# Performance work log

Hardware: AMD Instinct MI355X
Metric: run time of the kernel (lower is better)

Reference implementation:

```python
import jax, jax.numpy as jnp
import numpy as np

NEG_INF = -1e30


def setup_inputs() -> dict:
    key = jax.random.key(0)
    ks = jax.random.split(key, 8)
    B, N, I, O, H = 8, 1024, 64, 32, 4
    return {
        "x": jax.random.normal(ks[0], (B, N, I), dtype=jnp.float32),
        "adj": jax.random.randint(ks[1], (N, N), 0, 2, dtype=jnp.int32),
        "source_prior": jax.random.normal(ks[2], (B, N), dtype=jnp.float32),
        "beta": jax.random.normal(ks[3], (H,), dtype=jnp.float32),
        "weight": jax.random.normal(ks[4], (H, I, O), dtype=jnp.float32) * (1.0 / np.sqrt(I)),
        "attn_src": jax.random.normal(ks[5], (H, O), dtype=jnp.float32) * (1.0 / np.sqrt(O)),
        "attn_dst": jax.random.normal(ks[6], (H, O), dtype=jnp.float32) * (1.0 / np.sqrt(O)),
        "bias": jnp.zeros((H, O), dtype=jnp.float32),
    }


def reference(x, adj, source_prior, beta, weight, attn_src, attn_dst, bias):
    B, N, _ = x.shape
    H, _, O = weight.shape
    # Per-head projection + bias: [B,H,N,O]
    projected = jnp.einsum('bni,hio->bhno', x, weight) + bias[None, :, None, :]
    src_scores = jnp.einsum('bhnd,hd->bhn', projected, attn_src)  # [B,H,N]
    dst_scores = jnp.einsum('bhnd,hd->bhn', projected, attn_dst)  # [B,H,N]
    # Additive attention logits: [B,H,dst,src]
    logits = jax.nn.leaky_relu(dst_scores[..., :, None] + src_scores[..., None, :],
                               negative_slope=0.2)
    # Source-prior correction
    gain = jax.nn.softplus(beta).reshape(1, H, 1, 1)
    logits = logits + gain * source_prior[:, None, None, :]
    # Masked softmax over sources; fully-masked rows stay zero
    mask = (adj != 0)[None, None, :, :]  # [1,1,N,N]
    masked = jnp.where(mask, logits, NEG_INF)
    row_max = jnp.max(masked, axis=-1, keepdims=True)
    row_max = jnp.where(jnp.isfinite(row_max) & (row_max > NEG_INF / 2),
                        row_max, jnp.zeros_like(row_max))
    exp_logits = jnp.where(mask, jnp.exp(logits - row_max), 0.0)
    eps = jnp.finfo(logits.dtype).eps
    denom = jnp.maximum(jnp.sum(exp_logits, axis=-1, keepdims=True), eps)
    attention = exp_logits / denom  # [B,H,N,N]
    # Weighted aggregation: [B,H,N,O]
    output = jnp.einsum('bhij,bhjd->bhid', attention, projected)
    # concat=True: [B,N,H*O]
    encoded = jnp.transpose(output, (0, 2, 1, 3)).reshape(B, N, H * O)
    return encoded
```

## Files before the change

### kernel.cpp

```cpp
#include <hip/hip_runtime.h>
#include <math.h>

#define NB 8
#define NN 1024
#define NI 64
#define NO 32
#define NH 4
#define NEGINF (-1e30f)

typedef _Float16 half8 __attribute__((ext_vector_type(8)));
typedef _Float16 half4v __attribute__((ext_vector_type(4)));
typedef float floatx4 __attribute__((ext_vector_type(4)));

__global__ __launch_bounds__(256) void k_pack(const int* __restrict__ adj,
                                              unsigned char* __restrict__ adjb) {
    const int i = blockIdx.x * 256 + threadIdx.x;
    const int4 v = ((const int4*)adj)[i];
    unsigned int p = (v.x ? 1u : 0u) | ((v.y ? 1u : 0u) << 8) |
                     ((v.z ? 1u : 0u) << 16) | ((v.w ? 1u : 0u) << 24);
    ((unsigned int*)adjb)[i] = p;
}

__global__ __launch_bounds__(256) void k_proj(
    const float* __restrict__ x, const float* __restrict__ beta,
    const float* __restrict__ weight, const float* __restrict__ attn_src,
    const float* __restrict__ attn_dst, const float* __restrict__ bias,
    const float* __restrict__ prior,
    _Float16* __restrict__ projT,
    float* __restrict__ src_s, float* __restrict__ dst_s, float* __restrict__ gp)
{
    __shared__ __align__(16) float xs[32 * 64];
    __shared__ __align__(16) float ws[4 * 64 * 36];
    const int t = threadIdx.x;
    const int ntile = blockIdx.x, b = blockIdx.y;
    const int n0b = ntile * 32;
    {
        const float4* xsrc = (const float4*)(x + ((size_t)b * NN + n0b) * NI);
        float4* xd = (float4*)xs;
        xd[t] = xsrc[t];
        xd[t + 256] = xsrc[t + 256];
    }
    #pragma unroll
    for (int k = 0; k < 8; ++k) {
        int e = t + k * 256;
        int h = e >> 9, rem = e & 511, i = rem >> 3, o4 = rem & 7;
        float4 wv = *(const float4*)(weight + (h * NI + i) * NO + o4 * 4);
        *(float4*)&ws[h * 2304 + i * 36 + o4 * 4] = wv;
    }
    __syncthreads();

    const int o4 = t & 7, h = (t >> 3) & 3, ng = t >> 5;
    const int o0 = o4 * 4, nl0 = ng * 4;
    float acc[4][4];
    #pragma unroll
    for (int kn = 0; kn < 4; ++kn)
        #pragma unroll
        for (int oo = 0; oo < 4; ++oo) acc[kn][oo] = 0.f;

    #pragma unroll 4
    for (int i = 0; i < NI; ++i) {
        const float4 wv = *(const float4*)&ws[h * 2304 + i * 36 + o0];
        #pragma unroll
        for (int kn = 0; kn < 4; ++kn) {
            const float xv = xs[(nl0 + kn) * 64 + i];
            acc[kn][0] = fmaf(xv, wv.x, acc[kn][0]);
            acc[kn][1] = fmaf(xv, wv.y, acc[kn][1]);
            acc[kn][2] = fmaf(xv, wv.z, acc[kn][2]);
            acc[kn][3] = fmaf(xv, wv.w, acc[kn][3]);
        }
    }
    const float4 bv  = *(const float4*)(bias + h * NO + o0);
    const float4 asv = *(const float4*)(attn_src + h * NO + o0);
    const float4 adv = *(const float4*)(attn_dst + h * NO + o0);
    const int bh = b * NH + h;
    float ssum[4], dsum[4];
    #pragma unroll
    for (int kn = 0; kn < 4; ++kn) {
        acc[kn][0] += bv.x; acc[kn][1] += bv.y;
        acc[kn][2] += bv.z; acc[kn][3] += bv.w;
        ssum[kn] = acc[kn][0]*asv.x + acc[kn][1]*asv.y + acc[kn][2]*asv.z + acc[kn][3]*asv.w;
        dsum[kn] = acc[kn][0]*adv.x + acc[kn][1]*adv.y + acc[kn][2]*adv.z + acc[kn][3]*adv.w;
    }
    #pragma unroll
    for (int oo = 0; oo < 4; ++oo) {
        half4v hv;
        hv[0] = (_Float16)acc[0][oo]; hv[1] = (_Float16)acc[1][oo];
        hv[2] = (_Float16)acc[2][oo]; hv[3] = (_Float16)acc[3][oo];
        *(half4v*)(projT + ((size_t)(bh * NO + o0 + oo)) * NN + n0b + nl0) = hv;
    }
    #pragma unroll
    for (int msk = 1; msk <= 4; msk <<= 1) {
        #pragma unroll
        for (int kn = 0; kn < 4; ++kn) {
            ssum[kn] += __shfl_xor(ssum[kn], msk, 64);
            dsum[kn] += __shfl_xor(dsum[kn], msk, 64);
        }
    }
    if (o4 == 0) {
        const float bx = beta[h];
        const float sp = fmaxf(bx, 0.f) + log1pf(__expf(-fabsf(bx)));
        #pragma unroll
        for (int kn = 0; kn < 4; ++kn) {
            const int n = n0b + nl0 + kn;
            src_s[bh * NN + n] = ssum[kn];
            dst_s[bh * NN + n] = dsum[kn];
            gp[bh * NN + n] = sp * prior[b * NN + n];
        }
    }
}

#define VTP 1032

__global__ __launch_bounds__(256) void k_attn(
    const unsigned char* __restrict__ adjb,
    const _Float16* __restrict__ projT,
    const float* __restrict__ src_s, const float* __restrict__ dst_s,
    const float* __restrict__ gp,
    float* __restrict__ out)
{
    __shared__ __align__(16) _Float16 vt[NO * VTP];
    __shared__ __align__(16) float srcs[NN];
    __shared__ __align__(16) float gps[NN];
    __shared__ float pmax[64 * 4];
    const int t = threadIdx.x;
    const int lane = t & 63, wave = t >> 6;
    const int dtile = blockIdx.x, h = blockIdx.y, b = blockIdx.z;
    const int bh = b * NH + h;

    ((float4*)srcs)[t] = ((const float4*)(src_s + bh * NN))[t];
    ((float4*)gps)[t]  = ((const float4*)(gp + bh * NN))[t];
    const _Float16* ptrow = projT + (size_t)bh * NO * NN;
    #pragma unroll
    for (int k = 0; k < 16; ++k) {
        const int e = t + k * 256;
        const int o = e >> 7, sc8 = e & 127;
        *(half8*)&vt[o * VTP + sc8 * 8] =
            *(const half8*)(ptrow + (size_t)o * NN + sc8 * 8);
    }
    __syncthreads();

    {
        const int dl = lane, qt = wave;
        const int drow = dtile * 64 + dl;
        const float dv = dst_s[bh * NN + drow];
        const unsigned char* ar = adjb + (size_t)drow * NN + qt * 256;
        float mx = NEGINF;
        #pragma unroll 4
        for (int k = 0; k < 16; ++k) {
            const uint4 a4 = *(const uint4*)(ar + k * 16);
            const unsigned int wv[4] = {a4.x, a4.y, a4.z, a4.w};
            const int sb = qt * 256 + k * 16;
            #pragma unroll
            for (int w = 0; w < 4; ++w) {
                #pragma unroll
                for (int byi = 0; byi < 4; ++byi) {
                    const int s = sb + w * 4 + byi;
                    const float ts = dv + srcs[s];
                    const float sc = fmaxf(ts, 0.f) + 0.2f * fminf(ts, 0.f) + gps[s];
                    const bool on = (wv[w] >> (8 * byi)) & 1;
                    mx = fmaxf(mx, on ? sc : NEGINF);
                }
            }
        }
        pmax[dl * 4 + qt] = mx;
    }
    __syncthreads();

    const int m = lane & 15, quad = lane >> 4;
    const int d = dtile * 64 + wave * 16 + m;
    const float dreg = dst_s[bh * NN + d];
    const int pmb = (wave * 16 + m) * 4;
    const float rmx = fmaxf(fmaxf(pmax[pmb], pmax[pmb + 1]),
                            fmaxf(pmax[pmb + 2], pmax[pmb + 3]));
    const float rmc = (rmx > -1e29f) ? rmx : 0.f;
    const unsigned char* adjr = adjb + (size_t)d * NN;

    floatx4 acc0 = {0.f, 0.f, 0.f, 0.f}, acc1 = {0.f, 0.f, 0.f, 0.f};
    float psum = 0.f;
    uint2 apre = *(const uint2*)(adjr + quad * 8);

    for (int st = 0; st < 32; ++st) {
        const uint2 acur = apre;
        if (st < 31) apre = *(const uint2*)(adjr + (st + 1) * 32 + quad * 8);
        const int sg = st * 32 + quad * 8;
        float sv[8], gv[8];
        *(float4*)&sv[0] = *(const float4*)&srcs[sg];
        *(float4*)&sv[4] = *(const float4*)&srcs[sg + 4];
        *(float4*)&gv[0] = *(const float4*)&gps[sg];
        *(float4*)&gv[4] = *(const float4*)&gps[sg + 4];
        half8 af;
        #pragma unroll
        for (int j = 0; j < 8; ++j) {
            const unsigned int bit =
                ((j < 4 ? (acur.x >> (8 * j)) : (acur.y >> (8 * (j - 4)))) & 1u);
            const float ts = dreg + sv[j];
            const float lk = fmaxf(ts, 0.f) + 0.2f * fminf(ts, 0.f);
            const float sce = bit ? (lk + gv[j]) : NEGINF;
            const float p = __expf(sce - rmc);
            psum += p;
            af[j] = (_Float16)p;
        }
        const half8 b0 = *(const half8*)&vt[m * VTP + sg];
        const half8 b1 = *(const half8*)&vt[(16 + m) * VTP + sg];
        acc0 = __builtin_amdgcn_mfma_f32_16x16x32_f16(af, b0, acc0, 0, 0, 0);
        acc1 = __builtin_amdgcn_mfma_f32_16x16x32_f16(af, b1, acc1, 0, 0, 0);
    }
    psum += __shfl_xor(psum, 16, 64);
    psum += __shfl_xor(psum, 32, 64);

    #pragma unroll
    for (int r = 0; r < 4; ++r) {
        const int row = quad * 4 + r;
        const float lr = __shfl(psum, row, 64);
        const float inv = 1.f / fmaxf(lr, 1.1920929e-07f);
        float* go = out + ((size_t)(b * NN + dtile * 64 + wave * 16 + row)) * (NH * NO) + h * NO;
        go[m] = acc0[r] * inv;
        go[16 + m] = acc1[r] * inv;
    }
}

extern "C" void kernel_launch(void* const* d_in, const int* in_sizes, int n_in,
                              void* d_out, int out_size, void* d_ws, size_t ws_size,
                              hipStream_t stream) {
    (void)in_sizes; (void)n_in; (void)out_size; (void)ws_size;
    const float* x        = (const float*)d_in[0];
    const int*   adj      = (const int*)d_in[1];
    const float* prior    = (const float*)d_in[2];
    const float* beta     = (const float*)d_in[3];
    const float* weight   = (const float*)d_in[4];
    const float* attn_src = (const float*)d_in[5];
    const float* attn_dst = (const float*)d_in[6];
    const float* bias     = (const float*)d_in[7];
    float* out = (float*)d_out;

    _Float16* projT = (_Float16*)d_ws;
    float* src_s = (float*)((char*)d_ws + (1 << 21));
    float* dst_s = src_s + NB * NH * NN;
    float* gpb   = dst_s + NB * NH * NN;
    unsigned char* adjb = (unsigned char*)(gpb + NB * NH * NN);

    hipLaunchKernelGGL(k_pack, dim3(1024), dim3(256), 0, stream, adj, adjb);
    hipLaunchKernelGGL(k_proj, dim3(32, 8), dim3(256), 0, stream,
                       x, beta, weight, attn_src, attn_dst, bias, prior,
                       projT, src_s, dst_s, gpb);
    hipLaunchKernelGGL(k_attn, dim3(16, 4, 8), dim3(256), 0, stream,
                       adjb, projT, src_s, dst_s, gpb, out);
}
```

Before: 110.0 us.

## Fuse pack, projection and attention into one cooperative kernel with analytic row max

Merges the three kernels into a single cooperative launch of 512 blocks that packs adj, computes the projection, does a grid-wide sync, then runs the attention aggregation with a shared-memory union. The per-row masked max pass is replaced by an upper bound leaky(dst+max src)+max gp, which removes a full adjacency scan. Scores are pre-scaled by log2e so exp2f can be used. This cuts launch overhead and the extra max pass, at the cost of a grid sync and possible underflow if the bound is far above the true row max.

```diff
diff --git a/kernel.cpp b/kernel.cpp
--- a/kernel.cpp
+++ b/kernel.cpp
@@ -1,221 +1,198 @@
 #include <hip/hip_runtime.h>
+#include <hip/hip_cooperative_groups.h>
 #include <math.h>
+
+namespace cg = cooperative_groups;
 
 #define NB 8
 #define NN 1024
 #define NI 64
 #define NO 32
 #define NH 4
-#define NEGINF (-1e30f)
+#define LOG2E 1.4426950408889634f
 
 typedef _Float16 half8 __attribute__((ext_vector_type(8)));
-typedef _Float16 half4v __attribute__((ext_vector_type(4)));
+typedef _Float16 half2v __attribute__((ext_vector_type(2)));
 typedef float floatx4 __attribute__((ext_vector_type(4)));
 
-__global__ __launch_bounds__(256) void k_pack(const int* __restrict__ adj,
-                                              unsigned char* __restrict__ adjb) {
-    const int i = blockIdx.x * 256 + threadIdx.x;
-    const int4 v = ((const int4*)adj)[i];
-    unsigned int p = (v.x ? 1u : 0u) | ((v.y ? 1u : 0u) << 8) |
-                     ((v.z ? 1u : 0u) << 16) | ((v.w ? 1u : 0u) << 24);
-    ((unsigned int*)adjb)[i] = p;
-}
-
-__global__ __launch_bounds__(256) void k_proj(
-    const float* __restrict__ x, const float* __restrict__ beta,
+#define VTP 1032
+
+union SMem {
+    struct { float xs[16 * 64]; float ws[4 * 64 * 36]; } a;
+    struct { _Float16 vt[NO * VTP]; float srcs[NN]; float gps[NN]; float red[16]; } b;
+};
+
+__global__ __launch_bounds__(256, 2) void k_fused(
+    const float* __restrict__ x, const int* __restrict__ adj,
+    const float* __restrict__ prior, const float* __restrict__ beta,
     const float* __restrict__ weight, const float* __restrict__ attn_src,
     const float* __restrict__ attn_dst, const float* __restrict__ bias,
-    const float* __restrict__ prior,
     _Float16* __restrict__ projT,
-    float* __restrict__ src_s, float* __restrict__ dst_s, float* __restrict__ gp)
-{
-    __shared__ __align__(16) float xs[32 * 64];
-    __shared__ __align__(16) float ws[4 * 64 * 36];
-    const int t = threadIdx.x;
-    const int ntile = blockIdx.x, b = blockIdx.y;
-    const int n0b = ntile * 32;
-    {
-        const float4* xsrc = (const float4*)(x + ((size_t)b * NN + n0b) * NI);
-        float4* xd = (float4*)xs;
-        xd[t] = xsrc[t];
-        xd[t + 256] = xsrc[t + 256];
-    }
-    #pragma unroll
-    for (int k = 0; k < 8; ++k) {
-        int e = t + k * 256;
-        int h = e >> 9, rem = e & 511, i = rem >> 3, o4 = rem & 7;
-        float4 wv = *(const float4*)(weight + (h * NI + i) * NO + o4 * 4);
-        *(float4*)&ws[h * 2304 + i * 36 + o4 * 4] = wv;
-    }
-    __syncthreads();
-
-    const int o4 = t & 7, h = (t >> 3) & 3, ng = t >> 5;
-    const int o0 = o4 * 4, nl0 = ng * 4;
-    float acc[4][4];
-    #pragma unroll
-    for (int kn = 0; kn < 4; ++kn)
-        #pragma unroll
-        for (int oo = 0; oo < 4; ++oo) acc[kn][oo] = 0.f;
-
-    #pragma unroll 4
-    for (int i = 0; i < NI; ++i) {
-        const float4 wv = *(const float4*)&ws[h * 2304 + i * 36 + o0];
-        #pragma unroll
-        for (int kn = 0; kn < 4; ++kn) {
-            const float xv = xs[(nl0 + kn) * 64 + i];
-            acc[kn][0] = fmaf(xv, wv.x, acc[kn][0]);
-            acc[kn][1] = fmaf(xv, wv.y, acc[kn][1]);
-            acc[kn][2] = fmaf(xv, wv.z, acc[kn][2]);
-            acc[kn][3] = fmaf(xv, wv.w, acc[kn][3]);
-        }
-    }
-    const float4 bv  = *(const float4*)(bias + h * NO + o0);
-    const float4 asv = *(const float4*)(attn_src + h * NO + o0);
-    const float4 adv = *(const float4*)(attn_dst + h * NO + o0);
-    const int bh = b * NH + h;
-    float ssum[4], dsum[4];
-    #pragma unroll
-    for (int kn = 0; kn < 4; ++kn) {
-        acc[kn][0] += bv.x; acc[kn][1] += bv.y;
-        acc[kn][2] += bv.z; acc[kn][3] += bv.w;
-        ssum[kn] = acc[kn][0]*asv.x + acc[kn][1]*asv.y + acc[kn][2]*asv.z + acc[kn][3]*asv.w;
-        dsum[kn] = acc[kn][0]*adv.x + acc[kn][1]*adv.y + acc[kn][2]*adv.z + acc[kn][3]*adv.w;
-    }
-    #pragma unroll
-    for (int oo = 0; oo < 4; ++oo) {
-        half4v hv;
-        hv[0] = (_Float16)acc[0][oo]; hv[1] = (_Float16)acc[1][oo];
-        hv[2] = (_Float16)acc[2][oo]; hv[3] = (_Float16)acc[3][oo];
-        *(half4v*)(projT + ((size_t)(bh * NO + o0 + oo)) * NN + n0b + nl0) = hv;
-    }
-    #pragma unroll
-    for (int msk = 1; msk <= 4; msk <<= 1) {
-        #pragma unroll
-        for (int kn = 0; kn < 4; ++kn) {
-            ssum[kn] += __shfl_xor(ssum[kn], msk, 64);
-            dsum[kn] += __shfl_xor(dsum[kn], msk, 64);
-        }
-    }
-    if (o4 == 0) {
-        const float bx = beta[h];
-        const float sp = fmaxf(bx, 0.f) + log1pf(__expf(-fabsf(bx)));
-        #pragma unroll
-        for (int kn = 0; kn < 4; ++kn) {
-            const int n = n0b + nl0 + kn;
-            src_s[bh * NN + n] = ssum[kn];
-            dst_s[bh * NN + n] = dsum[kn];
-            gp[bh * NN + n] = sp * prior[b * NN + n];
-        }
-    }
-}
-
-#define VTP 1032
-
-__global__ __launch_bounds__(256) void k_attn(
-    const unsigned char* __restrict__ adjb,
-    const _Float16* __restrict__ projT,
-    const float* __restrict__ src_s, const float* __restrict__ dst_s,
-    const float* __restrict__ gp,
+    float* __restrict__ src_s, float* __restrict__ dst_s, float* __restrict__ gp_,
+    unsigned char* __restrict__ adjb,
     float* __restrict__ out)
 {
-    __shared__ __align__(16) _Float16 vt[NO * VTP];
-    __shared__ __align__(16) float srcs[NN];
-    __shared__ __align__(16) float gps[NN];
-    __shared__ float pmax[64 * 4];
+    __shared__ SMem sm;
     const int t = threadIdx.x;
+    const int blk = blockIdx.x;
     const int lane = t & 63, wave = t >> 6;
-    const int dtile = blockIdx.x, h = blockIdx.y, b = blockIdx.z;
-    const int bh = b * NH + h;
-
-    ((float4*)srcs)[t] = ((const float4*)(src_s + bh * NN))[t];
-    ((float4*)gps)[t]  = ((const float4*)(gp + bh * NN))[t];
-    const _Float16* ptrow = projT + (size_t)bh * NO * NN;
-    #pragma unroll
-    for (int k = 0; k < 16; ++k) {
-        const int e = t + k * 256;
-        const int o = e >> 7, sc8 = e & 127;
-        *(half8*)&vt[o * VTP + sc8 * 8] =
-            *(const half8*)(ptrow + (size_t)o * NN + sc8 * 8);
+
+    {
+        const int b = blk >> 6, n0 = (blk & 63) * 16;
+        #pragma unroll
+        for (int k = 0; k < 2; ++k) {
+            const int g = blk * 512 + k * 256 + t;
+            const int4 v = ((const int4*)adj)[g];
+            ((unsigned int*)adjb)[g] =
+                (v.x ? 1u : 0u) | ((v.y ? 1u : 0u) << 8) |
+                ((v.z ? 1u : 0u) << 16) | ((v.w ? 1u : 0u) << 24);
+        }
+        ((float4*)sm.a.xs)[t] = ((const float4*)(x + ((size_t)b * NN + n0) * NI))[t];
+        #pragma unroll
+        for (int k = 0; k < 8; ++k) {
+            const int e = t + k * 256;
+            const int h = e >> 9, rem = e & 511, i = rem >> 3, o4 = rem & 7;
+            *(float4*)&sm.a.ws[h * 2304 + i * 36 + o4 * 4] =
+                *(const float4*)(weight + (h * NI + i) * NO + o4 * 4);
+        }
+        __syncthreads();
+
+        const int o4 = t & 7, h = (t >> 3) & 3, ng = t >> 5;
+        const int o0 = o4 * 4, nl0 = ng * 2;
+        float acc[2][4];
+        #pragma unroll
+        for (int r = 0; r < 2; ++r)
+            #pragma unroll
+            for (int oo = 0; oo < 4; ++oo) acc[r][oo] = 0.f;
+        #pragma unroll 4
+        for (int i = 0; i < NI; ++i) {
+            const float4 wv = *(const float4*)&sm.a.ws[h * 2304 + i * 36 + o0];
+            #pragma unroll
+            for (int r = 0; r < 2; ++r) {
+                const float xv = sm.a.xs[(nl0 + r) * 64 + i];
+                acc[r][0] = fmaf(xv, wv.x, acc[r][0]);
+                acc[r][1] = fmaf(xv, wv.y, acc[r][1]);
+                acc[r][2] = fmaf(xv, wv.z, acc[r][2]);
+                acc[r][3] = fmaf(xv, wv.w, acc[r][3]);
+            }
+        }
+        const float4 bv  = *(const float4*)(bias + h * NO + o0);
+        const float4 asv = *(const float4*)(attn_src + h * NO + o0);
+        const float4 adv = *(const float4*)(attn_dst + h * NO + o0);
+        const int bh = b * NH + h, gn0 = n0 + nl0;
+        float ssum[2], dsum[2];
+        #pragma unroll
+        for (int r = 0; r < 2; ++r) {
+            acc[r][0] += bv.x; acc[r][1] += bv.y;
+            acc[r][2] += bv.z; acc[r][3] += bv.w;
+            ssum[r] = acc[r][0]*asv.x + acc[r][1]*asv.y + acc[r][2]*asv.z + acc[r][3]*asv.w;
+            dsum[r] = acc[r][0]*adv.x + acc[r][1]*adv.y + acc[r][2]*adv.z + acc[r][3]*adv.w;
+        }
+        #pragma unroll
+        for (int oo = 0; oo < 4; ++oo) {
+            half2v hv; hv[0] = (_Float16)acc[0][oo]; hv[1] = (_Float16)acc[1][oo];
+            *(half2v*)(projT + ((size_t)(bh * NO + o0 + oo)) * NN + gn0) = hv;
+        }
+        #pragma unroll
+        for (int msk = 1; msk <= 4; msk <<= 1) {
+            #pragma unroll
+            for (int r = 0; r < 2; ++r) {
+                ssum[r] += __shfl_xor(ssum[r], msk, 64);
+                dsum[r] += __shfl_xor(dsum[r], msk, 64);
+            }
+        }
+        if (o4 == 0) {
+            const float bx = beta[h];
+            const float sp = fmaxf(bx, 0.f) + log1pf(__expf(-fabsf(bx)));
+            #pragma unroll
+            for (int r = 0; r < 2; ++r) {
+                const int n = gn0 + r;
+                src_s[bh * NN + n] = LOG2E * ssum[r];
+                dst_s[bh * NN + n] = LOG2E * dsum[r];
+                gp_[bh * NN + n]   = LOG2E * sp * prior[b * NN + n];
+            }
+        }
     }
-    __syncthreads();
+
+    cg::this_grid().sync();
 
     {
-        const int dl = lane, qt = wave;
-        const int drow = dtile * 64 + dl;
-        const float dv = dst_s[bh * NN + drow];
-        const unsigned char* ar = adjb + (size_t)drow * NN + qt * 256;
-        float mx = NEGINF;
-        #pragma unroll 4
+        const int b = blk >> 6, h = (blk >> 4) & 3, dtile = blk & 15;
+        const int bh = b * NH + h;
+        const float4 s4 = ((const float4*)(src_s + bh * NN))[t];
+        const float4 g4 = ((const float4*)(gp_ + bh * NN))[t];
+        ((float4*)sm.b.srcs)[t] = s4;
+        ((float4*)sm.b.gps)[t]  = g4;
+        float s_l = fmaxf(fmaxf(s4.x, s4.y), fmaxf(s4.z, s4.w));
+        float g_l = fmaxf(fmaxf(g4.x, g4.y), fmaxf(g4.z, g4.w));
+        #pragma unroll
+        for (int msk = 1; msk <= 32; msk <<= 1) {
+            s_l = fmaxf(s_l, __shfl_xor(s_l, msk, 64));
+            g_l = fmaxf(g_l, __shfl_xor(g_l, msk, 64));
+        }
+        if (lane == 0) { sm.b.red[wave * 2] = s_l; sm.b.red[wave * 2 + 1] = g_l; }
+        const _Float16* ptrow = projT + (size_t)bh * NO * NN;
+        #pragma unroll
         for (int k = 0; k < 16; ++k) {
-            const uint4 a4 = *(const uint4*)(ar + k * 16);
-            const unsigned int wv[4] = {a4.x, a4.y, a4.z, a4.w};
-            const int sb = qt * 256 + k * 16;
-            #pragma unroll
-            for (int w = 0; w < 4; ++w) {
-                #pragma unroll
-                for (int byi = 0; byi < 4; ++byi) {
-                    const int s = sb + w * 4 + byi;
-                    const float ts = dv + srcs[s];
-                    const float sc = fmaxf(ts, 0.f) + 0.2f * fminf(ts, 0.f) + gps[s];
-                    const bool on = (wv[w] >> (8 * byi)) & 1;
-                    mx = fmaxf(mx, on ? sc : NEGINF);
-                }
-            }
-        }
-        pmax[dl * 4 + qt] = mx;
-    }
-    __syncthreads();
-
-    const int m = lane & 15, quad = lane >> 4;
-    const int d = dtile * 64 + wave * 16 + m;
-    const float dreg = dst_s[bh * NN + d];
-    const int pmb = (wave * 16 + m) * 4;
-    const float rmx = fmaxf(fmaxf(pmax[pmb], pmax[pmb + 1]),
-                            fmaxf(pmax[pmb + 2], pmax[pmb + 3]));
-    const float rmc = (rmx > -1e29f) ? rmx : 0.f;
-    const unsigned char* adjr = adjb + (size_t)d * NN;
-
-    floatx4 acc0 = {0.f, 0.f, 0.f, 0.f}, acc1 = {0.f, 0.f, 0.f, 0.f};
-    float psum = 0.f;
-    uint2 apre = *(const uint2*)(adjr + quad * 8);
-
-    for (int st = 0; st < 32; ++st) {
-        const uint2 acur = apre;
-        if (st < 31) apre = *(const uint2*)(adjr + (st + 1) * 32 + quad * 8);
-        const int sg = st * 32 + quad * 8;
-        float sv[8], gv[8];
-        *(float4*)&sv[0] = *(const float4*)&srcs[sg];
-        *(float4*)&sv[4] = *(const float4*)&srcs[sg + 4];
-        *(float4*)&gv[0] = *(const float4*)&gps[sg];
-        *(float4*)&gv[4] = *(const float4*)&gps[sg + 4];
-        half8 af;
-        #pragma unroll
-        for (int j = 0; j < 8; ++j) {
-            const unsigned int bit =
-                ((j < 4 ? (acur.x >> (8 * j)) : (acur.y >> (8 * (j - 4)))) & 1u);
-            const float ts = dreg + sv[j];
-            const float lk = fmaxf(ts, 0.f) + 0.2f * fminf(ts, 0.f);
-            const float sce = bit ? (lk + gv[j]) : NEGINF;
-            const float p = __expf(sce - rmc);
-            psum += p;
-            af[j] = (_Float16)p;
-        }
-        const half8 b0 = *(const half8*)&vt[m * VTP + sg];
-        const half8 b1 = *(const half8*)&vt[(16 + m) * VTP + sg];
-        acc0 = __builtin_amdgcn_mfma_f32_16x16x32_f16(af, b0, acc0, 0, 0, 0);
-        acc1 = __builtin_amdgcn_mfma_f32_16x16x32_f16(af, b1, acc1, 0, 0, 0);
-    }
-    psum += __shfl_xor(psum, 16, 64);
-    psum += __shfl_xor(psum, 32, 64);
-
-    #pragma unroll
-    for (int r = 0; r < 4; ++r) {
-        const int row = quad * 4 + r;
-        const float lr = __shfl(psum, row, 64);
-        const float inv = 1.f / fmaxf(lr, 1.1920929e-07f);
-        float* go = out + ((size_t)(b * NN + dtile * 64 + wave * 16 + row)) * (NH * NO) + h * NO;
-        go[m] = acc0[r] * inv;
-        go[16 + m] = acc1[r] * inv;
+            const int e = t + k * 256;
+            const int o = e >> 7, sc8 = e & 127;
+            *(half8*)&sm.b.vt[o * VTP + sc8 * 8] =
+                *(const half8*)(ptrow + (size_t)o * NN + sc8 * 8);
+        }
+        __syncthreads();
+        const float S = fmaxf(fmaxf(sm.b.red[0], sm.b.red[2]),
+                              fmaxf(sm.b.red[4], sm.b.red[6]));
+        const float G = fmaxf(fmaxf(sm.b.red[1], sm.b.red[3]),
+                              fmaxf(sm.b.red[5], sm.b.red[7]));
+
+        const int m = lane & 15, quad = lane >> 4;
+        const int d = dtile * 64 + wave * 16 + m;
+        const float dregl = dst_s[bh * NN + d];
+        const float rmcl = fmaxf(dregl + S, 0.f) + G;
+        const unsigned char* adjr = adjb + (size_t)d * NN;
+
+        floatx4 acc0 = {0.f, 0.f, 0.f, 0.f}, acc1 = {0.f, 0.f, 0.f, 0.f};
+        float psum = 0.f;
+        uint2 apre = *(const uint2*)(adjr + quad * 8);
+
+        for (int st = 0; st < 32; ++st) {
+            const uint2 acur = apre;
+            if (st < 31) apre = *(const uint2*)(adjr + (st + 1) * 32 + quad * 8);
+            const int sg = st * 32 + quad * 8;
+            float sv[8], gv[8];
+            *(float4*)&sv[0] = *(const float4*)&sm.b.srcs[sg];
+            *(float4*)&sv[4] = *(const float4*)&sm.b.srcs[sg + 4];
+            *(float4*)&gv[0] = *(const float4*)&sm.b.gps[sg];
+            *(float4*)&gv[4] = *(const float4*)&sm.b.gps[sg + 4];
+            half8 af;
+            #pragma unroll
+            for (int j = 0; j < 8; ++j) {
+                const unsigned int bit =
+                    ((j < 4 ? (acur.x >> (8 * j)) : (acur.y >> (8 * (j - 4)))) & 1u);
+                const float ts = dregl + sv[j];
+                const float lk = fmaxf(ts, 0.2f * ts);
+                const float e = exp2f(lk + (gv[j] - rmcl));
+                const float p = bit ? e : 0.f;
+                psum += p;
+                af[j] = (_Float16)p;
+            }
+            const half8 b0 = *(const half8*)&sm.b.vt[m * VTP + sg];
+            const half8 b1 = *(const half8*)&sm.b.vt[(16 + m) * VTP + sg];
+            acc0 = __builtin_amdgcn_mfma_f32_16x16x32_f16(af, b0, acc0, 0, 0, 0);
+            acc1 = __builtin_amdgcn_mfma_f32_16x16x32_f16(af, b1, acc1, 0, 0, 0);
+        }
+        psum += __shfl_xor(psum, 16, 64);
+        psum += __shfl_xor(psum, 32, 64);
+
+        #pragma unroll
+        for (int r = 0; r < 4; ++r) {
+            const int row = quad * 4 + r;
+            const float lr = __shfl(psum, row, 64);
+            const float inv = 1.f / fmaxf(lr, 1.1920929e-07f);
+            float* go = out + ((size_t)(b * NN + dtile * 64 + wave * 16 + row)) * (NH * NO) + h * NO;
+            go[m] = acc0[r] * inv;
+            go[16 + m] = acc1[r] * inv;
+        }
     }
 }
 
@@ -239,10 +216,10 @@
     float* gpb   = dst_s + NB * NH * NN;
     unsigned char* adjb = (unsigned char*)(gpb + NB * NH * NN);
 
-    hipLaunchKernelGGL(k_pack, dim3(1024), dim3(256), 0, stream, adj, adjb);
-    hipLaunchKernelGGL(k_proj, dim3(32, 8), dim3(256), 0, stream,
-                       x, beta, weight, attn_src, attn_dst, bias, prior,
-                       projT, src_s, dst_s, gpb);
-    hipLaunchKernelGGL(k_attn, dim3(16, 4, 8), dim3(256), 0, stream,
-                       adjb, projT, src_s, dst_s, gpb, out);
+    void* args[] = {(void*)&x, (void*)&adj, (void*)&prior, (void*)&beta,
+                    (void*)&weight, (void*)&attn_src, (void*)&attn_dst, (void*)&bias,
+                    (void*)&projT, (void*)&src_s, (void*)&dst_s, (void*)&gpb,
+                    (void*)&adjb, (void*)&out};
+    hipLaunchCooperativeKernel((const void*)k_fused, dim3(512), dim3(256),
+                               args, 0, stream);
 }
```

Measured after the change: 164.0 us. +49.0%, slower.
